# Kernel tuning notes

Measured on AMD Instinct MI355X. Metric: run time of the kernel, lower is better.

## Reference

```python
import jax, jax.numpy as jnp
import numpy as np

D = 64          # feature dim
H_POS = 64      # pos_mlp hidden
H_ATTN = 4 * D  # attn_mlp hidden
B, N = 1, 1024


def setup_inputs() -> dict:
    key = jax.random.key(0)
    ks = jax.random.split(key, 12)
    s = lambda fan_in: 1.0 / np.sqrt(fan_in)
    return {
        "x": jax.random.normal(ks[0], (B, N, D), jnp.float32),
        "pos": jax.random.normal(ks[1], (B, N, 2), jnp.float32),
        "Wq": jax.random.normal(ks[2], (D, D), jnp.float32) * s(D),
        "Wk": jax.random.normal(ks[3], (D, D), jnp.float32) * s(D),
        "Wv": jax.random.normal(ks[4], (D, D), jnp.float32) * s(D),
        "pW1": jax.random.normal(ks[5], (2, H_POS), jnp.float32) * s(2),
        "pb1": jnp.zeros((H_POS,), jnp.float32),
        "pW2": jax.random.normal(ks[6], (H_POS, D), jnp.float32) * s(H_POS),
        "pb2": jnp.zeros((D,), jnp.float32),
        "aW1": jax.random.normal(ks[7], (D, H_ATTN), jnp.float32) * s(D),
        "ab1": jnp.zeros((H_ATTN,), jnp.float32),
        "aW2": jax.random.normal(ks[8], (H_ATTN, D), jnp.float32) * s(H_ATTN),
        "ab2": jnp.zeros((D,), jnp.float32),
    }


def reference(x, pos, Wq, Wk, Wv, pW1, pb1, pW2, pb2, aW1, ab1, aW2, ab2):
    # projections: [b, n, d]
    q = x @ Wq
    k = x @ Wk
    v = x @ Wv
    # pairwise relative positions: [b, i, j, 2]
    rel_pos = pos[:, :, None, :] - pos[:, None, :, :]
    # pos MLP: [b, i, j, d]
    rpe = jax.nn.relu(rel_pos @ pW1 + pb1) @ pW2 + pb2
    # pairwise q - k: [b, i, j, d]
    qk_rel = q[:, :, None, :] - k[:, None, :, :]
    # values broadcast over i, plus positional embedding: [b, i, j, d]
    vv = v[:, None, :, :] + rpe
    # attention MLP on (qk_rel + rpe): [b, i, j, d]
    sim = jax.nn.relu((qk_rel + rpe) @ aW1 + ab1) @ aW2 + ab2
    # softmax over j (axis=-2), per-channel
    attn = jax.nn.softmax(sim, axis=-2)
    # weighted aggregation: [b, i, d]
    agg = jnp.einsum('bijd,bijd->bid', attn, vv)
    return agg
```

## Files before the change

### kernel.cpp

```cpp
#include <hip/hip_runtime.h>


typedef float f32x4 __attribute__((ext_vector_type(4)));
typedef int   i32x8 __attribute__((ext_vector_type(8)));
using sh8 = __attribute__((ext_vector_type(8))) short;

static constexpr int NPTS = 1024;

#if __has_builtin(__builtin_amdgcn_exp2f)
#define EXP2(x) __builtin_amdgcn_exp2f(x)
#else
#define EXP2(x) exp2f(x)
#endif

static constexpr size_t BEXT_OFF = 0;
static constexpr size_t AW2F_OFF = 65536;
static constexpr size_t PW2F_OFF = 98304;
static constexpr size_t CARR_OFF = 106496;
static constexpr size_t AI_OFF   = 107520;
static constexpr size_t VPT_OFF  = 369664;
static constexpr size_t AJ_OFF   = 631808;
static constexpr size_t KN_OFF   = 762880;
static constexpr size_t QA_OFF   = 893952;

__device__ __forceinline__ unsigned short f2b_rne(float f) {
    unsigned u = __float_as_uint(f);
    u += 0x7fffu + ((u >> 16) & 1u);
    return (unsigned short)(u >> 16);
}
__device__ __forceinline__ unsigned pk2(float lo, float hi) {
    return __builtin_amdgcn_perm(__float_as_uint(hi), __float_as_uint(lo), 0x07060302);
}
__device__ __forceinline__ float b2f(unsigned short s) {
    return __uint_as_float(((unsigned)s) << 16);
}
__device__ __forceinline__ unsigned char f2fp8(float v) {
    return (unsigned char)(__builtin_amdgcn_cvt_pk_fp8_f32(v, 0.f, 0, false) & 0xff);
}
__device__ __forceinline__ unsigned pk4fp8(float a, float b, float c, float d) {
    int r = __builtin_amdgcn_cvt_pk_fp8_f32(a, b, 0, false);
    r = __builtin_amdgcn_cvt_pk_fp8_f32(c, d, r, true);
    return (unsigned)r;
}
__device__ __forceinline__ i32x8 ld32B(const void* p) {
    const uint4 a = ((const uint4*)p)[0];
    const uint4 b = ((const uint4*)p)[1];
    i32x8 r;
    r[0] = a.x; r[1] = a.y; r[2] = a.z; r[3] = a.w;
    r[4] = b.x; r[5] = b.y; r[6] = b.z; r[7] = b.w;
    return r;
}

__global__ void prep_all(const float* __restrict__ x, const float* __restrict__ pos,
                         const float* __restrict__ Wq, const float* __restrict__ Wk,
                         const float* __restrict__ Wv, const float* __restrict__ pW1,
                         const float* __restrict__ pb1, const float* __restrict__ pW2,
                         const float* __restrict__ pb2, const float* __restrict__ aW1,
                         const float* __restrict__ ab1, const float* __restrict__ aW2,
                         unsigned short* __restrict__ bextf, unsigned char* __restrict__ aw2f8,
                         unsigned short* __restrict__ pw2f, float* __restrict__ cArr,
                         unsigned short* __restrict__ kN, float* __restrict__ vPT,
                         float* __restrict__ aI, unsigned short* __restrict__ aJ,
                         float* __restrict__ qa)
{
    __shared__ float s1[4][64];
    __shared__ float s2[4][64];
    const int b = blockIdx.x;
    if (b < 209) {
        const int idx = b * 256 + threadIdx.x;
        if (idx < 32768) {
            const int k = idx >> 8, t = idx & 255;
            float val;
            if (k < 64) {
                float s = 0.f;
                for (int d = 0; d < 64; ++d) s = fmaf(pW2[k * 64 + d], aW1[d * 256 + t], s);
                val = s;
            } else {
                val = aW1[(k - 64) * 256 + t];
            }
            const int kc = k >> 5, kl = k & 31, qq = kl >> 3, e = kl & 7;
            const int ntg = t >> 4, tl = t & 15;
            bextf[(((size_t)(kc * 16 + ntg) * 64) + (qq * 16 + tl)) * 8 + e] = f2b_rne(val);
        } else if (idx < 49152) {
            const int r = idx - 32768;
            const int e = r & 31, lane = (r >> 5) & 63, wsl = (r >> 11) & 3, kb = r >> 13;
            const int q = lane >> 4, dl = lane & 15;
            const int kp = kb * 128 + q * 32 + e;
            const int t = 64 * (kp >> 6) + 16 * (kp & 3) + ((kp >> 2) & 15);
            const int d = 16 * wsl + dl;
            aw2f8[r] = f2fp8(aW2[t * 64 + d] * 1.4426950408889634f);
        } else if (idx < 53248) {
            const int r = idx - 49152;
            const int k = r >> 6, d = r & 63;
            const int kc = k >> 5, kl = k & 31, qq = kl >> 3, e = kl & 7;
            const int nt = d >> 4, dl = d & 15;
            pw2f[(((size_t)(kc * 4 + nt) * 64) + (qq * 16 + dl)) * 8 + e] = f2b_rne(pW2[k * 64 + d]);
        } else if (idx < 53504) {
            const int t = idx - 53248;
            float s = ab1[t];
            for (int d = 0; d < 64; ++d) s = fmaf(pb2[d], aW1[d * 256 + t], s);
            cArr[t] = s;
        }
    } else if (b < 465) {
        const int t = threadIdx.x, sub = t >> 6, d = t & 63;
        const int i = (b - 209) * 4 + sub;
        s1[sub][d] = x[i * 64 + d];
        __syncthreads();
        float k = 0.f, v = 0.f;
        for (int e = 0; e < 64; ++e) {
            const float xe = s1[sub][e];
            k = fmaf(xe, Wk[e * 64 + d], k);
            v = fmaf(xe, Wv[e * 64 + d], v);
        }
        const float a = pos[i * 2] * pW1[d] + pos[i * 2 + 1] * pW1[64 + d];
        kN[i * 64 + d] = f2b_rne(-k);
        vPT[d * NPTS + i] = v + pb2[d];
        aI[i * 64 + d] = a + pb1[d];
        aJ[i * 64 + d] = f2b_rne(a);
    } else {
        const int i = b - 465, t = threadIdx.x;
        if (t < 64) s1[0][t] = x[i * 64 + t];
        __syncthreads();
        if (t < 64) {
            float s = 0.f;
            for (int e = 0; e < 64; ++e) s = fmaf(s1[0][e], Wq[e * 64 + t], s);
            s2[0][t] = s;
        }
        __syncthreads();
        float s = 0.f;
        for (int d = 0; d < 64; ++d) s = fmaf(s2[0][d], aW1[d * 256 + t], s);
        qa[(size_t)i * 256 + t] = s;
    }
}

__global__ __launch_bounds__(256, 2) void ptl_main(
    const float* __restrict__ aI, const unsigned short* __restrict__ aJ,
    const unsigned short* __restrict__ kN, const float* __restrict__ vPT,
    const unsigned short* __restrict__ bextf, const unsigned char* __restrict__ aw2f8,
    const unsigned short* __restrict__ pw2f, const float* __restrict__ cArr,
    const float* __restrict__ qa, float* __restrict__ out)
{
    const int i    = blockIdx.x;
    const int tid  = threadIdx.x;
    const int w    = tid >> 6;
    const int lane = tid & 63;
    const int m    = lane & 15;
    const int q    = lane >> 4;

    __shared__ __align__(16) uint4 AfL[2][2][4][64];
    __shared__ __align__(16) unsigned char Hs[2][2][16 * 272];

    sh8 Bf[16];
#pragma unroll
    for (int kc = 0; kc < 4; ++kc)
#pragma unroll
        for (int nt = 0; nt < 4; ++nt)
            Bf[kc * 4 + nt] = *(const sh8*)(bextf + ((size_t)((kc * 16 + 4 * w + nt) * 64 + lane)) * 8);
    i32x8 W2f[2];
#pragma unroll
    for (int kb = 0; kb < 2; ++kb)
        W2f[kb] = ld32B(aw2f8 + ((size_t)((kb * 4 + w) * 64 + lane)) * 32);
    sh8 P2f[2];
#pragma unroll
    for (int kc = 0; kc < 2; ++kc)
        P2f[kc] = *(const sh8*)(pw2f + ((size_t)((kc * 4 + w) * 64 + lane)) * 8);

    float creg[4];
#pragma unroll
    for (int nt = 0; nt < 4; ++nt)
        creg[nt] = cArr[64 * w + 16 * nt + m] + qa[(size_t)i * 256 + 64 * w + 16 * nt + m];

    const int s_ = w >> 1, h_ = w & 1;
    const unsigned short* bsrcA = aJ + m * 64 + h_ * 32 + q * 8;
    const unsigned short* bsrcK = kN + m * 64 + h_ * 32 + q * 8;
    const float*          ibase = aI + (size_t)i * 64 + h_ * 32 + q * 8;
    float iv[8];
    *(float4*)(iv)     = *(const float4*)(ibase);
    *(float4*)(iv + 4) = *(const float4*)(ibase + 4);

    {
        const sh8  rawA = *(const sh8*)(bsrcA + (size_t)(16 * s_) * 64);
        const uint4 rawK = *(const uint4*)(bsrcK + (size_t)(16 * s_) * 64);
        float t[8];
#pragma unroll
        for (int e = 0; e < 8; ++e)
            t[e] = fmaxf(iv[e] - b2f((unsigned short)rawA[e]), 0.f);
        uint4 pk;
        pk.x = pk2(t[0], t[1]); pk.y = pk2(t[2], t[3]);
        pk.z = pk2(t[4], t[5]); pk.w = pk2(t[6], t[7]);
        AfL[0][s_][h_][lane]     = pk;
        AfL[0][s_][2 + h_][lane] = rawK;
    }
    __syncthreads();

    float num = 0.f, den = 0.f;
    const f32x4 z4 = {0.f, 0.f, 0.f, 0.f};
    f32x4 aRp0 = z4, aRp1 = z4;
    const float* vbase = vPT + (size_t)(16 * w + m) * NPTS;

    for (int n = 0; n < 32; ++n) {
        const int pb = n & 1, nb = pb ^ 1;
        const int j0 = n << 5;

        sh8  rawA;
        uint4 rawK;
        if (n < 31) {
            rawA = *(const sh8*)(bsrcA + (size_t)(j0 + 32 + 16 * s_) * 64);
            rawK = *(const uint4*)(bsrcK + (size_t)(j0 + 32 + 16 * s_) * 64);
        }
        const float4 vj0 = *(const float4*)(vbase + j0 + 4 * q);
        const float4 vj1 = *(const float4*)(vbase + j0 + 16 + 4 * q);

        const sh8 A00 = *(const sh8*)&AfL[pb][0][0][lane];
        const sh8 A01 = *(const sh8*)&AfL[pb][0][1][lane];
        const sh8 A02 = *(const sh8*)&AfL[pb][0][2][lane];
        const sh8 A03 = *(const sh8*)&AfL[pb][0][3][lane];
        {
            f32x4 acc[4];
#pragma unroll
            for (int nt = 0; nt < 4; ++nt) {
                const f32x4 cv = {creg[nt], creg[nt], creg[nt], creg[nt]};
                acc[nt] = __builtin_amdgcn_mfma_f32_16x16x32_bf16(A00, Bf[0 * 4 + nt], cv, 0, 0, 0);
                acc[nt] = __builtin_amdgcn_mfma_f32_16x16x32_bf16(A01, Bf[1 * 4 + nt], acc[nt], 0, 0, 0);
                acc[nt] = __builtin_amdgcn_mfma_f32_16x16x32_bf16(A02, Bf[2 * 4 + nt], acc[nt], 0, 0, 0);
                acc[nt] = __builtin_amdgcn_mfma_f32_16x16x32_bf16(A03, Bf[3 * 4 + nt], acc[nt], 0, 0, 0);
            }
            unsigned char* hw = Hs[pb][0] + (4 * q) * 272 + 64 * w + 4 * m;
#pragma unroll
            for (int r = 0; r < 4; ++r)
                *(unsigned*)(hw + r * 272) = pk4fp8(fmaxf(acc[0][r], 0.f), fmaxf(acc[1][r], 0.f),
                                                   fmaxf(acc[2][r], 0.f), fmaxf(acc[3][r], 0.f));
        }

        i32x8 h00, h01, h10, h11;
        if (n) {
            h00 = ld32B(Hs[nb][0] + m * 272 + 0   + 32 * q);
            h01 = ld32B(Hs[nb][0] + m * 272 + 128 + 32 * q);
            h10 = ld32B(Hs[nb][1] + m * 272 + 0   + 32 * q);
            h11 = ld32B(Hs[nb][1] + m * 272 + 128 + 32 * q);
        }

        const sh8 A10 = *(const sh8*)&AfL[pb][1][0][lane];
        const sh8 A11 = *(const sh8*)&AfL[pb][1][1][lane];
        const sh8 A12 = *(const sh8*)&AfL[pb][1][2][lane];
        const sh8 A13 = *(const sh8*)&AfL[pb][1][3][lane];
        {
            f32x4 acc[4];
#pragma unroll
            for (int nt = 0; nt < 4; ++nt) {
                const f32x4 cv = {creg[nt], creg[nt], creg[nt], creg[nt]};
                acc[nt] = __builtin_amdgcn_mfma_f32_16x16x32_bf16(A10, Bf[0 * 4 + nt], cv, 0, 0, 0);
                acc[nt] = __builtin_amdgcn_mfma_f32_16x16x32_bf16(A11, Bf[1 * 4 + nt], acc[nt], 0, 0, 0);
                acc[nt] = __builtin_amdgcn_mfma_f32_16x16x32_bf16(A12, Bf[2 * 4 + nt], acc[nt], 0, 0, 0);
                acc[nt] = __builtin_amdgcn_mfma_f32_16x16x32_bf16(A13, Bf[3 * 4 + nt], acc[nt], 0, 0, 0);
            }
            unsigned char* hw = Hs[pb][1] + (4 * q) * 272 + 64 * w + 4 * m;
#pragma unroll
            for (int r = 0; r < 4; ++r)
                *(unsigned*)(hw + r * 272) = pk4fp8(fmaxf(acc[0][r], 0.f), fmaxf(acc[1][r], 0.f),
                                                   fmaxf(acc[2][r], 0.f), fmaxf(acc[3][r], 0.f));
        }

        if (n) {
            f32x4 aS0 = z4, aS1 = z4;
            aS0 = __builtin_amdgcn_mfma_scale_f32_16x16x128_f8f6f4(
                h00, W2f[0], aS0, 0, 0, 0, 127, 0, 127);
            aS0 = __builtin_amdgcn_mfma_scale_f32_16x16x128_f8f6f4(
                h01, W2f[1], aS0, 0, 0, 0, 127, 0, 127);
            aS1 = __builtin_amdgcn_mfma_scale_f32_16x16x128_f8f6f4(
                h10, W2f[0], aS1, 0, 0, 0, 127, 0, 127);
            aS1 = __builtin_amdgcn_mfma_scale_f32_16x16x128_f8f6f4(
                h11, W2f[1], aS1, 0, 0, 0, 127, 0, 127);
#pragma unroll
            for (int r = 0; r < 4; ++r) {
                const float e0 = EXP2(aS0[r]);
                num = fmaf(e0, aRp0[r], num);
                den += e0;
                const float e1 = EXP2(aS1[r]);
                num = fmaf(e1, aRp1[r], num);
                den += e1;
            }
        }

        const f32x4 vc0 = {vj0.x, vj0.y, vj0.z, vj0.w};
        const f32x4 vc1 = {vj1.x, vj1.y, vj1.z, vj1.w};
        f32x4 aR0 = __builtin_amdgcn_mfma_f32_16x16x32_bf16(A00, P2f[0], vc0, 0, 0, 0);
        aR0 = __builtin_amdgcn_mfma_f32_16x16x32_bf16(A01, P2f[1], aR0, 0, 0, 0);
        f32x4 aR1 = __builtin_amdgcn_mfma_f32_16x16x32_bf16(A10, P2f[0], vc1, 0, 0, 0);
        aR1 = __builtin_amdgcn_mfma_f32_16x16x32_bf16(A11, P2f[1], aR1, 0, 0, 0);
        aRp0 = aR0;
        aRp1 = aR1;

        if (n < 31) {
            float t[8];
#pragma unroll
            for (int e = 0; e < 8; ++e)
                t[e] = fmaxf(iv[e] - b2f((unsigned short)rawA[e]), 0.f);
            uint4 pk;
            pk.x = pk2(t[0], t[1]); pk.y = pk2(t[2], t[3]);
            pk.z = pk2(t[4], t[5]); pk.w = pk2(t[6], t[7]);
            AfL[nb][s_][h_][lane]     = pk;
            AfL[nb][s_][2 + h_][lane] = rawK;
        }

        __syncthreads();
    }

    {
        f32x4 aS0 = z4, aS1 = z4;
        const i32x8 h00 = ld32B(Hs[1][0] + m * 272 + 0   + 32 * q);
        const i32x8 h01 = ld32B(Hs[1][0] + m * 272 + 128 + 32 * q);
        const i32x8 h10 = ld32B(Hs[1][1] + m * 272 + 0   + 32 * q);
        const i32x8 h11 = ld32B(Hs[1][1] + m * 272 + 128 + 32 * q);
        aS0 = __builtin_amdgcn_mfma_scale_f32_16x16x128_f8f6f4(
            h00, W2f[0], aS0, 0, 0, 0, 127, 0, 127);
        aS0 = __builtin_amdgcn_mfma_scale_f32_16x16x128_f8f6f4(
            h01, W2f[1], aS0, 0, 0, 0, 127, 0, 127);
        aS1 = __builtin_amdgcn_mfma_scale_f32_16x16x128_f8f6f4(
            h10, W2f[0], aS1, 0, 0, 0, 127, 0, 127);
        aS1 = __builtin_amdgcn_mfma_scale_f32_16x16x128_f8f6f4(
            h11, W2f[1], aS1, 0, 0, 0, 127, 0, 127);
#pragma unroll
        for (int r = 0; r < 4; ++r) {
            const float e0 = EXP2(aS0[r]);
            num = fmaf(e0, aRp0[r], num);
            den += e0;
            const float e1 = EXP2(aS1[r]);
            num = fmaf(e1, aRp1[r], num);
            den += e1;
        }
    }

    num += __shfl_xor(num, 16);
    num += __shfl_xor(num, 32);
    den += __shfl_xor(den, 16);
    den += __shfl_xor(den, 32);
    if (q == 0) out[i * 64 + 16 * w + m] = num / den;
}

extern "C" void kernel_launch(void* const* d_in, const int* in_sizes, int n_in,
                              void* d_out, int out_size, void* d_ws, size_t ws_size,
                              hipStream_t stream) {
    const float* x   = (const float*)d_in[0];
    const float* pos = (const float*)d_in[1];
    const float* Wq  = (const float*)d_in[2];
    const float* Wk  = (const float*)d_in[3];
    const float* Wv  = (const float*)d_in[4];
    const float* pW1 = (const float*)d_in[5];
    const float* pb1 = (const float*)d_in[6];
    const float* pW2 = (const float*)d_in[7];
    const float* pb2 = (const float*)d_in[8];
    const float* aW1 = (const float*)d_in[9];
    const float* ab1 = (const float*)d_in[10];
    const float* aW2 = (const float*)d_in[11];

    char* ws = (char*)d_ws;
    unsigned short* bextf = (unsigned short*)(ws + BEXT_OFF);
    unsigned char*  aw2f8 = (unsigned char*)(ws + AW2F_OFF);
    unsigned short* pw2f  = (unsigned short*)(ws + PW2F_OFF);
    float*          cArr  = (float*)(ws + CARR_OFF);
    float*          aIa   = (float*)(ws + AI_OFF);
    float*          vPTa  = (float*)(ws + VPT_OFF);
    unsigned short* aJa   = (unsigned short*)(ws + AJ_OFF);
    unsigned short* kNa   = (unsigned short*)(ws + KN_OFF);
    float*          qaA   = (float*)(ws + QA_OFF);

    prep_all<<<1489, 256, 0, stream>>>(x, pos, Wq, Wk, Wv, pW1, pb1, pW2, pb2, aW1, ab1, aW2,
                                       bextf, aw2f8, pw2f, cArr, kNa, vPTa, aIa, aJa, qaA);
    ptl_main<<<NPTS, 256, 0, stream>>>(aIa, aJa, kNa, vPTa, bextf, aw2f8, pw2f, cArr, qaA,
                                       (float*)d_out);
}
```

Measured before the change: 175.1 us.

## Run first attention-MLP layer in FP8 with scaled 16x16x128 MFMA

Moves the first attention-MLP GEMM (relu(rel-pos hidden) and -k concatenated against [pW2·aW1; aW1]) from four bf16 16x16x32 MFMAs per tile to a single FP8 16x16x128 scaled MFMA. The extended weight and kN are now prepared as FP8, and an extra FP8 LDS staging buffer holds the A fragments while bf16 fragments are kept for the positional product. This cuts MFMA issue count, register use for B fragments and global traffic for kN. The cost is lower precision in the pre-ReLU activations plus extra conversion and LDS writes per tile.

After: 159.7 us (median of 2 runs). 1.1x faster.

```diff
diff --git a/kernel.cpp b/kernel.cpp
--- a/kernel.cpp
+++ b/kernel.cpp
@@ -13,15 +13,15 @@
 #define EXP2(x) exp2f(x)
 #endif
 
-static constexpr size_t BEXT_OFF = 0;
-static constexpr size_t AW2F_OFF = 65536;
-static constexpr size_t PW2F_OFF = 98304;
-static constexpr size_t CARR_OFF = 106496;
-static constexpr size_t AI_OFF   = 107520;
-static constexpr size_t VPT_OFF  = 369664;
-static constexpr size_t AJ_OFF   = 631808;
-static constexpr size_t KN_OFF   = 762880;
-static constexpr size_t QA_OFF   = 893952;
+static constexpr size_t BEXT8_OFF = 0;
+static constexpr size_t AW2F_OFF = 32768;
+static constexpr size_t PW2F_OFF = 49152;
+static constexpr size_t CARR_OFF = 57344;
+static constexpr size_t AI_OFF   = 58368;
+static constexpr size_t VPT_OFF  = 320512;
+static constexpr size_t AJ_OFF   = 582656;
+static constexpr size_t KN8_OFF  = 713728;
+static constexpr size_t QA_OFF   = 779264;
 
 __device__ __forceinline__ unsigned short f2b_rne(float f) {
     unsigned u = __float_as_uint(f);
@@ -57,50 +57,50 @@
                          const float* __restrict__ pb1, const float* __restrict__ pW2,
                          const float* __restrict__ pb2, const float* __restrict__ aW1,
                          const float* __restrict__ ab1, const float* __restrict__ aW2,
-                         unsigned short* __restrict__ bextf, unsigned char* __restrict__ aw2f8,
+                         unsigned char* __restrict__ bext8, unsigned char* __restrict__ aw2f8,
                          unsigned short* __restrict__ pw2f, float* __restrict__ cArr,
-                         unsigned short* __restrict__ kN, float* __restrict__ vPT,
+                         unsigned char* __restrict__ kN8, float* __restrict__ vPT,
                          float* __restrict__ aI, unsigned short* __restrict__ aJ,
                          float* __restrict__ qa)
 {
     __shared__ float s1[4][64];
     __shared__ float s2[4][64];
     const int b = blockIdx.x;
-    if (b < 209) {
-        const int idx = b * 256 + threadIdx.x;
-        if (idx < 32768) {
-            const int k = idx >> 8, t = idx & 255;
-            float val;
-            if (k < 64) {
-                float s = 0.f;
-                for (int d = 0; d < 64; ++d) s = fmaf(pW2[k * 64 + d], aW1[d * 256 + t], s);
-                val = s;
-            } else {
-                val = aW1[(k - 64) * 256 + t];
-            }
-            const int kc = k >> 5, kl = k & 31, qq = kl >> 3, e = kl & 7;
-            const int ntg = t >> 4, tl = t & 15;
-            bextf[(((size_t)(kc * 16 + ntg) * 64) + (qq * 16 + tl)) * 8 + e] = f2b_rne(val);
-        } else if (idx < 49152) {
-            const int r = idx - 32768;
-            const int e = r & 31, lane = (r >> 5) & 63, wsl = (r >> 11) & 3, kb = r >> 13;
-            const int q = lane >> 4, dl = lane & 15;
-            const int kp = kb * 128 + q * 32 + e;
-            const int t = 64 * (kp >> 6) + 16 * (kp & 3) + ((kp >> 2) & 15);
-            const int d = 16 * wsl + dl;
-            aw2f8[r] = f2fp8(aW2[t * 64 + d] * 1.4426950408889634f);
-        } else if (idx < 53248) {
-            const int r = idx - 49152;
-            const int k = r >> 6, d = r & 63;
-            const int kc = k >> 5, kl = k & 31, qq = kl >> 3, e = kl & 7;
-            const int nt = d >> 4, dl = d & 15;
-            pw2f[(((size_t)(kc * 4 + nt) * 64) + (qq * 16 + dl)) * 8 + e] = f2b_rne(pW2[k * 64 + d]);
-        } else if (idx < 53504) {
-            const int t = idx - 53248;
-            float s = ab1[t];
-            for (int d = 0; d < 64; ++d) s = fmaf(pb2[d], aW1[d * 256 + t], s);
-            cArr[t] = s;
-        }
+    if (b < 128) {
+        const int r = b * 256 + threadIdx.x;
+        const int frag = r >> 11, lane = (r >> 5) & 63, e = r & 31;
+        const int w = frag >> 2, nt = frag & 3;
+        const int tl = lane & 15, qq = lane >> 4;
+        const int k = qq * 32 + e;
+        const int t = 64 * w + 16 * nt + tl;
+        float val;
+        if (k < 64) {
+            float s = 0.f;
+            for (int d = 0; d < 64; ++d) s = fmaf(pW2[k * 64 + d], aW1[d * 256 + t], s);
+            val = s;
+        } else {
+            val = aW1[(k - 64) * 256 + t];
+        }
+        bext8[r] = f2fp8(val);
+    } else if (b < 192) {
+        const int r = (b - 128) * 256 + threadIdx.x;
+        const int e = r & 31, lane = (r >> 5) & 63, wsl = (r >> 11) & 3, kb = r >> 13;
+        const int q = lane >> 4, dl = lane & 15;
+        const int kp = kb * 128 + q * 32 + e;
+        const int t = 64 * (kp >> 6) + 16 * (kp & 3) + ((kp >> 2) & 15);
+        const int d = 16 * wsl + dl;
+        aw2f8[r] = f2fp8(aW2[t * 64 + d] * 1.4426950408889634f);
+    } else if (b < 208) {
+        const int r = (b - 192) * 256 + threadIdx.x;
+        const int k = r >> 6, d = r & 63;
+        const int kc = k >> 5, kl = k & 31, qq = kl >> 3, e = kl & 7;
+        const int nt = d >> 4, dl = d & 15;
+        pw2f[(((size_t)(kc * 4 + nt) * 64) + (qq * 16 + dl)) * 8 + e] = f2b_rne(pW2[k * 64 + d]);
+    } else if (b == 208) {
+        const int t = threadIdx.x;
+        float s = ab1[t];
+        for (int d = 0; d < 64; ++d) s = fmaf(pb2[d], aW1[d * 256 + t], s);
+        cArr[t] = s;
     } else if (b < 465) {
         const int t = threadIdx.x, sub = t >> 6, d = t & 63;
         const int i = (b - 209) * 4 + sub;
@@ -113,7 +113,7 @@
             v = fmaf(xe, Wv[e * 64 + d], v);
         }
         const float a = pos[i * 2] * pW1[d] + pos[i * 2 + 1] * pW1[64 + d];
-        kN[i * 64 + d] = f2b_rne(-k);
+        kN8[i * 64 + d] = f2fp8(-k);
         vPT[d * NPTS + i] = v + pb2[d];
         aI[i * 64 + d] = a + pb1[d];
         aJ[i * 64 + d] = f2b_rne(a);
@@ -135,8 +135,8 @@
 
 __global__ __launch_bounds__(256, 2) void ptl_main(
     const float* __restrict__ aI, const unsigned short* __restrict__ aJ,
-    const unsigned short* __restrict__ kN, const float* __restrict__ vPT,
-    const unsigned short* __restrict__ bextf, const unsigned char* __restrict__ aw2f8,
+    const unsigned char* __restrict__ kN8, const float* __restrict__ vPT,
+    const unsigned char* __restrict__ bext8, const unsigned char* __restrict__ aw2f8,
     const unsigned short* __restrict__ pw2f, const float* __restrict__ cArr,
     const float* __restrict__ qa, float* __restrict__ out)
 {
@@ -147,15 +147,14 @@
     const int m    = lane & 15;
     const int q    = lane >> 4;
 
-    __shared__ __align__(16) uint4 AfL[2][2][4][64];
+    __shared__ __align__(16) uint4 AfL[2][2][2][64];
+    __shared__ __align__(16) unsigned char Af8[2][2][16 * 144];
     __shared__ __align__(16) unsigned char Hs[2][2][16 * 272];
 
-    sh8 Bf[16];
-#pragma unroll
-    for (int kc = 0; kc < 4; ++kc)
-#pragma unroll
-        for (int nt = 0; nt < 4; ++nt)
-            Bf[kc * 4 + nt] = *(const sh8*)(bextf + ((size_t)((kc * 16 + 4 * w + nt) * 64 + lane)) * 8);
+    i32x8 B8f[4];
+#pragma unroll
+    for (int nt = 0; nt < 4; ++nt)
+        B8f[nt] = ld32B(bext8 + ((size_t)((4 * w + nt) * 64 + lane)) * 32);
     i32x8 W2f[2];
 #pragma unroll
     for (int kb = 0; kb < 2; ++kb)
@@ -171,16 +170,16 @@
         creg[nt] = cArr[64 * w + 16 * nt + m] + qa[(size_t)i * 256 + 64 * w + 16 * nt + m];
 
     const int s_ = w >> 1, h_ = w & 1;
-    const unsigned short* bsrcA = aJ + m * 64 + h_ * 32 + q * 8;
-    const unsigned short* bsrcK = kN + m * 64 + h_ * 32 + q * 8;
-    const float*          ibase = aI + (size_t)i * 64 + h_ * 32 + q * 8;
+    const unsigned short* bsrcA  = aJ  + m * 64 + h_ * 32 + q * 8;
+    const unsigned char*  bsrcK8 = kN8 + m * 64 + h_ * 32 + q * 8;
+    const float*          ibase  = aI + (size_t)i * 64 + h_ * 32 + q * 8;
     float iv[8];
     *(float4*)(iv)     = *(const float4*)(ibase);
     *(float4*)(iv + 4) = *(const float4*)(ibase + 4);
 
     {
-        const sh8  rawA = *(const sh8*)(bsrcA + (size_t)(16 * s_) * 64);
-        const uint4 rawK = *(const uint4*)(bsrcK + (size_t)(16 * s_) * 64);
+        const sh8  rawA  = *(const sh8*)(bsrcA + (size_t)(16 * s_) * 64);
+        const uint2 rawK = *(const uint2*)(bsrcK8 + (size_t)(16 * s_) * 64);
         float t[8];
 #pragma unroll
         for (int e = 0; e < 8; ++e)
@@ -188,8 +187,12 @@
         uint4 pk;
         pk.x = pk2(t[0], t[1]); pk.y = pk2(t[2], t[3]);
         pk.z = pk2(t[4], t[5]); pk.w = pk2(t[6], t[7]);
-        AfL[0][s_][h_][lane]     = pk;
-        AfL[0][s_][2 + h_][lane] = rawK;
+        AfL[0][s_][h_][lane] = pk;
+        uint2 f8;
+        f8.x = pk4fp8(t[0], t[1], t[2], t[3]);
+        f8.y = pk4fp8(t[4], t[5], t[6], t[7]);
+        *(uint2*)(Af8[0][s_] + m * 144 + h_ * 32 + q * 8)      = f8;
+        *(uint2*)(Af8[0][s_] + m * 144 + 64 + h_ * 32 + q * 8) = rawK;
     }
     __syncthreads();
 
@@ -203,27 +206,22 @@
         const int j0 = n << 5;
 
         sh8  rawA;
-        uint4 rawK;
+        uint2 rawK;
         if (n < 31) {
             rawA = *(const sh8*)(bsrcA + (size_t)(j0 + 32 + 16 * s_) * 64);
-            rawK = *(const uint4*)(bsrcK + (size_t)(j0 + 32 + 16 * s_) * 64);
+            rawK = *(const uint2*)(bsrcK8 + (size_t)(j0 + 32 + 16 * s_) * 64);
         }
         const float4 vj0 = *(const float4*)(vbase + j0 + 4 * q);
         const float4 vj1 = *(const float4*)(vbase + j0 + 16 + 4 * q);
 
-        const sh8 A00 = *(const sh8*)&AfL[pb][0][0][lane];
-        const sh8 A01 = *(const sh8*)&AfL[pb][0][1][lane];
-        const sh8 A02 = *(const sh8*)&AfL[pb][0][2][lane];
-        const sh8 A03 = *(const sh8*)&AfL[pb][0][3][lane];
         {
+            const i32x8 A8 = ld32B(Af8[pb][0] + m * 144 + 32 * q);
             f32x4 acc[4];
 #pragma unroll
             for (int nt = 0; nt < 4; ++nt) {
                 const f32x4 cv = {creg[nt], creg[nt], creg[nt], creg[nt]};
-                acc[nt] = __builtin_amdgcn_mfma_f32_16x16x32_bf16(A00, Bf[0 * 4 + nt], cv, 0, 0, 0);
-                acc[nt] = __builtin_amdgcn_mfma_f32_16x16x32_bf16(A01, Bf[1 * 4 + nt], acc[nt], 0, 0, 0);
-                acc[nt] = __builtin_amdgcn_mfma_f32_16x16x32_bf16(A02, Bf[2 * 4 + nt], acc[nt], 0, 0, 0);
-                acc[nt] = __builtin_amdgcn_mfma_f32_16x16x32_bf16(A03, Bf[3 * 4 + nt], acc[nt], 0, 0, 0);
+                acc[nt] = __builtin_amdgcn_mfma_scale_f32_16x16x128_f8f6f4(
+                    A8, B8f[nt], cv, 0, 0, 0, 127, 0, 127);
             }
             unsigned char* hw = Hs[pb][0] + (4 * q) * 272 + 64 * w + 4 * m;
 #pragma unroll
@@ -240,19 +238,14 @@
             h11 = ld32B(Hs[nb][1] + m * 272 + 128 + 32 * q);
         }
 
-        const sh8 A10 = *(const sh8*)&AfL[pb][1][0][lane];
-        const sh8 A11 = *(const sh8*)&AfL[pb][1][1][lane];
-        const sh8 A12 = *(const sh8*)&AfL[pb][1][2][lane];
-        const sh8 A13 = *(const sh8*)&AfL[pb][1][3][lane];
         {
+            const i32x8 A8 = ld32B(Af8[pb][1] + m * 144 + 32 * q);
             f32x4 acc[4];
 #pragma unroll
             for (int nt = 0; nt < 4; ++nt) {
                 const f32x4 cv = {creg[nt], creg[nt], creg[nt], creg[nt]};
-                acc[nt] = __builtin_amdgcn_mfma_f32_16x16x32_bf16(A10, Bf[0 * 4 + nt], cv, 0, 0, 0);
-                acc[nt] = __builtin_amdgcn_mfma_f32_16x16x32_bf16(A11, Bf[1 * 4 + nt], acc[nt], 0, 0, 0);
-                acc[nt] = __builtin_amdgcn_mfma_f32_16x16x32_bf16(A12, Bf[2 * 4 + nt], acc[nt], 0, 0, 0);
-                acc[nt] = __builtin_amdgcn_mfma_f32_16x16x32_bf16(A13, Bf[3 * 4 + nt], acc[nt], 0, 0, 0);
+                acc[nt] = __builtin_amdgcn_mfma_scale_f32_16x16x128_f8f6f4(
+                    A8, B8f[nt], cv, 0, 0, 0, 127, 0, 127);
             }
             unsigned char* hw = Hs[pb][1] + (4 * q) * 272 + 64 * w + 4 * m;
 #pragma unroll
@@ -260,6 +253,11 @@
                 *(unsigned*)(hw + r * 272) = pk4fp8(fmaxf(acc[0][r], 0.f), fmaxf(acc[1][r], 0.f),
                                                    fmaxf(acc[2][r], 0.f), fmaxf(acc[3][r], 0.f));
         }
+
+        const sh8 A00 = *(const sh8*)&AfL[pb][0][0][lane];
+        const sh8 A01 = *(const sh8*)&AfL[pb][0][1][lane];
+        const sh8 A10 = *(const sh8*)&AfL[pb][1][0][lane];
+        const sh8 A11 = *(const sh8*)&AfL[pb][1][1][lane];
 
         if (n) {
             f32x4 aS0 = z4, aS1 = z4;
@@ -299,8 +297,12 @@
             uint4 pk;
             pk.x = pk2(t[0], t[1]); pk.y = pk2(t[2], t[3]);
             pk.z = pk2(t[4], t[5]); pk.w = pk2(t[6], t[7]);
-            AfL[nb][s_][h_][lane]     = pk;
-            AfL[nb][s_][2 + h_][lane] = rawK;
+            AfL[nb][s_][h_][lane] = pk;
+            uint2 f8;
+            f8.x = pk4fp8(t[0], t[1], t[2], t[3]);
+            f8.y = pk4fp8(t[4], t[5], t[6], t[7]);
+            *(uint2*)(Af8[nb][s_] + m * 144 + h_ * 32 + q * 8)      = f8;
+            *(uint2*)(Af8[nb][s_] + m * 144 + 64 + h_ * 32 + q * 8) = rawK;
         }
 
         __syncthreads();
@@ -355,18 +357,18 @@
     const float* aW2 = (const float*)d_in[11];
 
     char* ws = (char*)d_ws;
-    unsigned short* bextf = (unsigned short*)(ws + BEXT_OFF);
+    unsigned char*  bext8 = (unsigned char*)(ws + BEXT8_OFF);
     unsigned char*  aw2f8 = (unsigned char*)(ws + AW2F_OFF);
     unsigned short* pw2f  = (unsigned short*)(ws + PW2F_OFF);
     float*          cArr  = (float*)(ws + CARR_OFF);
     float*          aIa   = (float*)(ws + AI_OFF);
     float*          vPTa  = (float*)(ws + VPT_OFF);
     unsigned short* aJa   = (unsigned short*)(ws + AJ_OFF);
-    unsigned short* kNa   = (unsigned short*)(ws + KN_OFF);
+    unsigned char*  kN8a  = (unsigned char*)(ws + KN8_OFF);
     float*          qaA   = (float*)(ws + QA_OFF);
 
     prep_all<<<1489, 256, 0, stream>>>(x, pos, Wq, Wk, Wv, pW1, pb1, pW2, pb2, aW1, ab1, aW2,
-                                       bextf, aw2f8, pw2f, cArr, kNa, vPTa, aIa, aJa, qaA);
-    ptl_main<<<NPTS, 256, 0, stream>>>(aIa, aJa, kNa, vPTa, bextf, aw2f8, pw2f, cArr, qaA,
+                                       bext8, aw2f8, pw2f, cArr, kN8a, vPTa, aIa, aJa, qaA);
+    ptl_main<<<NPTS, 256, 0, stream>>>(aIa, aJa, kN8a, vPTa, bext8, aw2f8, pw2f, cArr, qaA,
                                        (float*)d_out);
 }
```
